# Kernel tuning notes

Hardware: AMD Instinct MI355X
Metric: run time of the kernel (lower is better)

The kernel has to match this reference:

```python
import jax, jax.numpy as jnp
import numpy as np

N_NODES = 100000
N_EDGES = 100000
D = 256
N_SIDE = 2  # rel_list = [side_a, side_b, rel_c, rel_d]
N_REL = 2


def setup_inputs() -> dict:
    key = jax.random.key(0)
    ks = jax.random.split(key, 7)
    h = jax.random.normal(ks[0], (N_NODES, D), dtype=jnp.float32)
    src_idx = jax.random.randint(ks[1], (N_SIDE + N_REL, N_EDGES), 0, N_NODES)
    dst_idx = jax.random.randint(ks[2], (N_SIDE + N_REL, N_EDGES), 0, N_NODES)
    # shared bilinear matrix R (nn.Linear(D, D, bias=False): y = x @ R_W.T)
    R_W = jax.random.normal(ks[3], (D, D), dtype=jnp.float32) * (1.0 / np.sqrt(D))
    # per-'side*' diagonal parameters (xavier over [D,1] then squeeze)
    d_side = jax.random.normal(ks[4], (N_SIDE, D), dtype=jnp.float32)
    # per-regular-relation Linear weights (with bias)
    W_rel = jax.random.normal(ks[5], (N_REL, D, D), dtype=jnp.float32) * (1.0 / np.sqrt(D))
    b_rel = jax.random.normal(ks[6], (N_REL, D), dtype=jnp.float32) * 0.01
    return {"h": h, "src_idx": src_idx, "dst_idx": dst_idx,
            "R_W": R_W, "d_side": d_side, "W_rel": W_rel, "b_rel": b_rel}


def reference(h, src_idx, dst_idx, R_W, d_side, W_rel, b_rel):
    # --- 'side*' edge types: score = (((h_u * d) @ R_W.T) * d) . h_v ---
    hu_s = h[src_idx[:N_SIDE]]            # [S, E, D] gather
    hv_s = h[dst_idx[:N_SIDE]]            # [S, E, D]
    lft = hu_s * d_side[:, None, :]       # [S, E, D]
    lft = jnp.einsum('sed,fd->sef', lft, R_W)  # Linear, no bias
    lft = lft * d_side[:, None, :]
    score_side = jnp.einsum('sed,sed->se', lft, hv_s)  # [S, E]

    # --- regular edge types: score = (h_u @ W.T + b) . h_v ---
    hu_r = h[src_idx[N_SIDE:]]            # [R, E, D]
    hv_r = h[dst_idx[N_SIDE:]]            # [R, E, D]
    lft_r = jnp.einsum('red,rfd->ref', hu_r, W_rel) + b_rel[:, None, :]
    score_rel = jnp.einsum('red,red->re', lft_r, hv_r)  # [R, E]

    return jnp.concatenate([score_side, score_rel], axis=0)  # [S+R, E]
```

## Files before the change

### kernel.cpp

```cpp
#include <hip/hip_runtime.h>
#include <stdint.h>

#define NNODES 100000
#define NEDGES 100000
#define DIM    256
#define NCH    4
#define ET     64
#define NT     1563
#define NBX    64
#define RSF    264
#define CONVB  2048

typedef _Float16 f16x8 __attribute__((ext_vector_type(8)));
typedef _Float16 f16x4 __attribute__((ext_vector_type(4)));
typedef float f32x4  __attribute__((ext_vector_type(4)));

__global__ void prep_fused(const float* __restrict__ RW,
                           const float* __restrict__ dside,
                           const float* __restrict__ Wrel,
                           const float* __restrict__ h,
                           _Float16* __restrict__ Bh, _Float16* __restrict__ Bl,
                           _Float16* __restrict__ H16) {
    if (blockIdx.x < 128) {
        int t = blockIdx.x * blockDim.x + threadIdx.x;
        int lane = t & 63;
        int ft   = (t >> 6) & 15;
        int kc   = (t >> 10) & 7;
        int c    = t >> 13;
        int quad = lane >> 4, col = lane & 15;
        int f     = ft * 16 + col;
        int kbase = kc * 32 + quad * 8;

        f16x8 vh, vl;
#pragma unroll
        for (int j = 0; j < 8; ++j) {
            int k = kbase + j;
            float val;
            if (c < 2) {
                val = dside[c * DIM + f] * RW[f * DIM + k] * dside[c * DIM + k];
            } else {
                val = Wrel[(size_t)(c - 2) * DIM * DIM + f * DIM + k];
            }
            _Float16 hi = (_Float16)val;
            vh[j] = hi;
            vl[j] = (_Float16)(val - (float)hi);
        }
        ((f16x8*)Bh)[t] = vh;
        ((f16x8*)Bl)[t] = vl;
    } else {
        const int total4 = NNODES * DIM / 4;
        const int stride = CONVB * 256;
        int i = (blockIdx.x - 128) * 256 + (int)threadIdx.x;
        const f32x4* s4 = (const f32x4*)h;
        f16x4* d4 = (f16x4*)H16;
        for (; i + stride < total4; i += 2 * stride) {
            f32x4 a = s4[i];
            f32x4 b = s4[i + stride];
            f16x4 oa, ob;
#pragma unroll
            for (int j = 0; j < 4; ++j) { oa[j] = (_Float16)a[j]; ob[j] = (_Float16)b[j]; }
            d4[i] = oa; d4[i + stride] = ob;
        }
        if (i < total4) {
            f32x4 a = s4[i];
            f16x4 o;
#pragma unroll
            for (int j = 0; j < 4; ++j) o[j] = (_Float16)a[j];
            d4[i] = o;
        }
    }
}

__device__ __forceinline__ float dpp_reduce16(float s) {
    union { float f; int i; } u, v;
    u.f = s; v.i = __builtin_amdgcn_update_dpp(0, u.i, 0xB1,  0xF, 0xF, true); s += v.f;
    u.f = s; v.i = __builtin_amdgcn_update_dpp(0, u.i, 0x4E,  0xF, 0xF, true); s += v.f;
    u.f = s; v.i = __builtin_amdgcn_update_dpp(0, u.i, 0x141, 0xF, 0xF, true); s += v.f;
    u.f = s; v.i = __builtin_amdgcn_update_dpp(0, u.i, 0x140, 0xF, 0xF, true); s += v.f;
    return s;
}

__global__ __launch_bounds__(512, 1)
void edge_kernel(const _Float16* __restrict__ H16,
                 const int* __restrict__ src_idx,
                 const int* __restrict__ dst_idx,
                 const float* __restrict__ brel,
                 const _Float16* __restrict__ Bh_sw,
                 const _Float16* __restrict__ Bl_sw,
                 float* __restrict__ out) {
    const int c    = blockIdx.y;
    const int tid  = threadIdx.x;
    const int w    = tid >> 6;
    const int lane = tid & 63;
    const int quad = lane >> 4, col = lane & 15;

    __shared__ __align__(16) _Float16 s_a[ET * RSF];
    __shared__ __align__(16) _Float16 s_v[ET * RSF];
    __shared__ float red[8][ET];

    f16x8 Bh_r[8][2], Bl_r[8][2];
    {
        const f16x8* bh = (const f16x8*)Bh_sw;
        const f16x8* bl = (const f16x8*)Bl_sw;
#pragma unroll
        for (int kc = 0; kc < 8; ++kc)
#pragma unroll
            for (int ftl = 0; ftl < 2; ++ftl) {
                int o = ((c * 8 + kc) * 16 + (w * 2 + ftl)) * 64 + lane;
                Bh_r[kc][ftl] = bh[o];
                Bl_r[kc][ftl] = bl[o];
            }
    }
#pragma unroll
    for (int kc = 0; kc < 8; ++kc)
#pragma unroll
        for (int ftl = 0; ftl < 2; ++ftl)
            asm volatile("" : "+v"(Bh_r[kc][ftl]), "+v"(Bl_r[kc][ftl]));

    float bias[2];
#pragma unroll
    for (int ftl = 0; ftl < 2; ++ftl) {
        int f = (w * 2 + ftl) * 16 + col;
        bias[ftl] = (c >= 2) ? brel[(size_t)(c - 2) * DIM + f] : 0.f;
    }

    const int  j8   = lane & 7;
    const bool isV  = (lane & 8) != 0;
    const int* ibase = (isV ? dst_idx : src_idx) + (size_t)c * NEDGES;

    auto loadpack = [&](int t) -> int {
        int e = t * ET + w * 8 + j8;
        if (e >= NEDGES) e = NEDGES - 1;
        return ibase[e];
    };

    const int t0 = blockIdx.x;
    f16x4 pA[8], pV[8];
    {
        int ip = loadpack(t0);
#pragma unroll
        for (int i = 0; i < 8; ++i) {
            int ia = __shfl(ip, i, 64);
            int iv = __shfl(ip, 8 + i, 64);
            pA[i] = *(const f16x4*)(H16 + (size_t)ia * DIM + lane * 4);
            pV[i] = *(const f16x4*)(H16 + (size_t)iv * DIM + lane * 4);
        }
    }
    int ipk0 = 0, ipk1 = 0;
    if (t0 + NBX < NT) ipk1 = loadpack(t0 + NBX);

    auto body = [&](int t, int& ipkUse, int& ipkLoad) {
#pragma unroll
        for (int i = 0; i < 8; ++i) {
            int lr = w * 8 + i;
            *(f16x4*)&s_a[lr * RSF + lane * 4] = pA[i];
            *(f16x4*)&s_v[lr * RSF + lane * 4] = pV[i];
        }
        __syncthreads();

        if (t + 2 * NBX < NT) ipkLoad = loadpack(t + 2 * NBX);
        if (t + NBX < NT) {
#pragma unroll
            for (int i = 0; i < 8; ++i) {
                int ia = __shfl(ipkUse, i, 64);
                int iv = __shfl(ipkUse, 8 + i, 64);
                pA[i] = *(const f16x4*)(H16 + (size_t)ia * DIM + lane * 4);
                pV[i] = *(const f16x4*)(H16 + (size_t)iv * DIM + lane * 4);
            }
        }

        f32x4 acc[4][2];
#pragma unroll
        for (int mt = 0; mt < 4; ++mt)
#pragma unroll
            for (int ftl = 0; ftl < 2; ++ftl) acc[mt][ftl] = (f32x4){0.f, 0.f, 0.f, 0.f};

#pragma unroll
        for (int kc = 0; kc < 8; ++kc) {
            f16x8 A[4];
#pragma unroll
            for (int mt = 0; mt < 4; ++mt)
                A[mt] = *(const f16x8*)&s_a[(mt * 16 + col) * RSF + kc * 32 + quad * 8];
#pragma unroll
            for (int ftl = 0; ftl < 2; ++ftl) {
#pragma unroll
                for (int mt = 0; mt < 4; ++mt)
                    acc[mt][ftl] = __builtin_amdgcn_mfma_f32_16x16x32_f16(A[mt], Bh_r[kc][ftl], acc[mt][ftl], 0, 0, 0);
#pragma unroll
                for (int mt = 0; mt < 4; ++mt)
                    acc[mt][ftl] = __builtin_amdgcn_mfma_f32_16x16x32_f16(A[mt], Bl_r[kc][ftl], acc[mt][ftl], 0, 0, 0);
            }
        }

        float psum[4][4];
#pragma unroll
        for (int mt = 0; mt < 4; ++mt) {
#pragma unroll
            for (int r = 0; r < 4; ++r) {
                int el = mt * 16 + quad * 4 + r;
                float s = 0.f;
#pragma unroll
                for (int ftl = 0; ftl < 2; ++ftl) {
                    int f = (w * 2 + ftl) * 16 + col;
                    float v = (float)s_v[el * RSF + f];
                    s += (acc[mt][ftl][r] + bias[ftl]) * v;
                }
                psum[mt][r] = dpp_reduce16(s);
            }
        }
        if (col == 0) {
#pragma unroll
            for (int mt = 0; mt < 4; ++mt)
#pragma unroll
                for (int r = 0; r < 4; ++r)
                    red[w][mt * 16 + quad * 4 + r] = psum[mt][r];
        }
        __syncthreads();

        if (tid < ET) {
            int e = t * ET + tid;
            if (e < NEDGES) {
                float s = 0.f;
#pragma unroll
                for (int i = 0; i < 8; ++i) s += red[i][tid];
                out[(size_t)c * NEDGES + e] = s;
            }
        }
    };

    int t = t0;
    while (true) {
        body(t, ipk1, ipk0);
        t += NBX; if (t >= NT) break;
        body(t, ipk0, ipk1);
        t += NBX; if (t >= NT) break;
    }
}

extern "C" void kernel_launch(void* const* d_in, const int* in_sizes, int n_in,
                              void* d_out, int out_size, void* d_ws, size_t ws_size,
                              hipStream_t stream) {
    const float* hmat  = (const float*)d_in[0];
    const int*   src   = (const int*)d_in[1];
    const int*   dst   = (const int*)d_in[2];
    const float* RW    = (const float*)d_in[3];
    const float* dside = (const float*)d_in[4];
    const float* Wrel  = (const float*)d_in[5];
    const float* brel  = (const float*)d_in[6];
    float* out = (float*)d_out;

    const size_t nB = (size_t)NCH * DIM * DIM;
    _Float16* Bh  = (_Float16*)d_ws;
    _Float16* Bl  = Bh + nB;
    _Float16* H16 = Bl + nB;

    prep_fused<<<dim3(128 + CONVB), dim3(256), 0, stream>>>(
        RW, dside, Wrel, hmat, Bh, Bl, H16);

    dim3 grid(NBX, NCH);
    edge_kernel<<<grid, dim3(512), 0, stream>>>(H16, src, dst, brel, Bh, Bl, out);
}
```

Baseline: 277.7 us.

## Double-buffer edge tiles and replace block reduction with atomic accumulation

The edge kernel now alternates between two LDS tile buffers, which drops one of the two block-wide barriers per iteration. The cross-wave reduction through shared memory is replaced by per-wave float atomicAdd into the output, which the prep kernel now zeroes first. Index broadcasts use readlane instead of shfl. The tradeoff is more global atomic traffic, a nondeterministic summation order, and twice the LDS footprint.

```diff
diff --git a/kernel.cpp b/kernel.cpp
--- a/kernel.cpp
+++ b/kernel.cpp
@@ -10,6 +10,7 @@
 #define NBX    64
 #define RSF    264
 #define CONVB  2048
+#define ZEROB  391
 
 typedef _Float16 f16x8 __attribute__((ext_vector_type(8)));
 typedef _Float16 f16x4 __attribute__((ext_vector_type(4)));
@@ -20,7 +21,8 @@
                            const float* __restrict__ Wrel,
                            const float* __restrict__ h,
                            _Float16* __restrict__ Bh, _Float16* __restrict__ Bl,
-                           _Float16* __restrict__ H16) {
+                           _Float16* __restrict__ H16,
+                           float* __restrict__ out) {
     if (blockIdx.x < 128) {
         int t = blockIdx.x * blockDim.x + threadIdx.x;
         int lane = t & 63;
@@ -47,10 +49,14 @@
         }
         ((f16x8*)Bh)[t] = vh;
         ((f16x8*)Bl)[t] = vl;
+    } else if (blockIdx.x < 128 + ZEROB) {
+        int i4 = (blockIdx.x - 128) * 256 + (int)threadIdx.x;
+        if (i4 < NCH * NEDGES / 4)
+            ((f32x4*)out)[i4] = (f32x4){0.f, 0.f, 0.f, 0.f};
     } else {
         const int total4 = NNODES * DIM / 4;
         const int stride = CONVB * 256;
-        int i = (blockIdx.x - 128) * 256 + (int)threadIdx.x;
+        int i = (blockIdx.x - 128 - ZEROB) * 256 + (int)threadIdx.x;
         const f32x4* s4 = (const f32x4*)h;
         f16x4* d4 = (f16x4*)H16;
         for (; i + stride < total4; i += 2 * stride) {
@@ -94,9 +100,10 @@
     const int lane = tid & 63;
     const int quad = lane >> 4, col = lane & 15;
 
-    __shared__ __align__(16) _Float16 s_a[ET * RSF];
-    __shared__ __align__(16) _Float16 s_v[ET * RSF];
-    __shared__ float red[8][ET];
+    __shared__ __align__(16) _Float16 s_a0[ET * RSF];
+    __shared__ __align__(16) _Float16 s_v0[ET * RSF];
+    __shared__ __align__(16) _Float16 s_a1[ET * RSF];
+    __shared__ __align__(16) _Float16 s_v1[ET * RSF];
 
     f16x8 Bh_r[8][2], Bl_r[8][2];
     {
@@ -140,8 +147,8 @@
         int ip = loadpack(t0);
 #pragma unroll
         for (int i = 0; i < 8; ++i) {
-            int ia = __shfl(ip, i, 64);
-            int iv = __shfl(ip, 8 + i, 64);
+            int ia = __builtin_amdgcn_readlane(ip, i);
+            int iv = __builtin_amdgcn_readlane(ip, 8 + i);
             pA[i] = *(const f16x4*)(H16 + (size_t)ia * DIM + lane * 4);
             pV[i] = *(const f16x4*)(H16 + (size_t)iv * DIM + lane * 4);
         }
@@ -149,26 +156,27 @@
     int ipk0 = 0, ipk1 = 0;
     if (t0 + NBX < NT) ipk1 = loadpack(t0 + NBX);
 
-    auto body = [&](int t, int& ipkUse, int& ipkLoad) {
+    auto body = [&](int t, _Float16* sa, _Float16* sv, int& ipkUse, int& ipkLoad) {
 #pragma unroll
         for (int i = 0; i < 8; ++i) {
             int lr = w * 8 + i;
-            *(f16x4*)&s_a[lr * RSF + lane * 4] = pA[i];
-            *(f16x4*)&s_v[lr * RSF + lane * 4] = pV[i];
-        }
-        __syncthreads();
+            *(f16x4*)&sa[lr * RSF + lane * 4] = pA[i];
+            *(f16x4*)&sv[lr * RSF + lane * 4] = pV[i];
+        }
 
         if (t + 2 * NBX < NT) ipkLoad = loadpack(t + 2 * NBX);
         if (t + NBX < NT) {
 #pragma unroll
             for (int i = 0; i < 8; ++i) {
-                int ia = __shfl(ipkUse, i, 64);
-                int iv = __shfl(ipkUse, 8 + i, 64);
+                int ia = __builtin_amdgcn_readlane(ipkUse, i);
+                int iv = __builtin_amdgcn_readlane(ipkUse, 8 + i);
                 pA[i] = *(const f16x4*)(H16 + (size_t)ia * DIM + lane * 4);
                 pV[i] = *(const f16x4*)(H16 + (size_t)iv * DIM + lane * 4);
             }
         }
 
+        __syncthreads();
+
         f32x4 acc[4][2];
 #pragma unroll
         for (int mt = 0; mt < 4; ++mt)
@@ -180,7 +188,7 @@
             f16x8 A[4];
 #pragma unroll
             for (int mt = 0; mt < 4; ++mt)
-                A[mt] = *(const f16x8*)&s_a[(mt * 16 + col) * RSF + kc * 32 + quad * 8];
+                A[mt] = *(const f16x8*)&sa[(mt * 16 + col) * RSF + kc * 32 + quad * 8];
 #pragma unroll
             for (int ftl = 0; ftl < 2; ++ftl) {
 #pragma unroll
@@ -192,9 +200,9 @@
             }
         }
 
-        float psum[4][4];
 #pragma unroll
         for (int mt = 0; mt < 4; ++mt) {
+            float ps[4];
 #pragma unroll
             for (int r = 0; r < 4; ++r) {
                 int el = mt * 16 + quad * 4 + r;
@@ -202,37 +210,27 @@
 #pragma unroll
                 for (int ftl = 0; ftl < 2; ++ftl) {
                     int f = (w * 2 + ftl) * 16 + col;
-                    float v = (float)s_v[el * RSF + f];
+                    float v = (float)sv[el * RSF + f];
                     s += (acc[mt][ftl][r] + bias[ftl]) * v;
                 }
-                psum[mt][r] = dpp_reduce16(s);
-            }
-        }
-        if (col == 0) {
-#pragma unroll
-            for (int mt = 0; mt < 4; ++mt)
-#pragma unroll
-                for (int r = 0; r < 4; ++r)
-                    red[w][mt * 16 + quad * 4 + r] = psum[mt][r];
-        }
-        __syncthreads();
-
-        if (tid < ET) {
-            int e = t * ET + tid;
-            if (e < NEDGES) {
-                float s = 0.f;
-#pragma unroll
-                for (int i = 0; i < 8; ++i) s += red[i][tid];
-                out[(size_t)c * NEDGES + e] = s;
+                ps[r] = dpp_reduce16(s);
+            }
+            if (col == 0) {
+#pragma unroll
+                for (int r = 0; r < 4; ++r) {
+                    int e = t * ET + mt * 16 + quad * 4 + r;
+                    if (e < NEDGES)
+                        atomicAdd(&out[(size_t)c * NEDGES + e], ps[r]);
+                }
             }
         }
     };
 
     int t = t0;
     while (true) {
-        body(t, ipk1, ipk0);
+        body(t, s_a0, s_v0, ipk1, ipk0);
         t += NBX; if (t >= NT) break;
-        body(t, ipk0, ipk1);
+        body(t, s_a1, s_v1, ipk0, ipk1);
         t += NBX; if (t >= NT) break;
     }
 }
@@ -254,8 +252,8 @@
     _Float16* Bl  = Bh + nB;
     _Float16* H16 = Bl + nB;
 
-    prep_fused<<<dim3(128 + CONVB), dim3(256), 0, stream>>>(
-        RW, dside, Wrel, hmat, Bh, Bl, H16);
+    prep_fused<<<dim3(128 + ZEROB + CONVB), dim3(256), 0, stream>>>(
+        RW, dside, Wrel, hmat, Bh, Bl, H16, out);
 
     dim3 grid(NBX, NCH);
     edge_kernel<<<grid, dim3(512), 0, stream>>>(H16, src, dst, brel, Bh, Bl, out);
```

New measurement: 290.3 us. 4.6% more time.

## Double-buffer LDS tiles with XOR swizzle and 16-byte gathers

Applied to the files above, without the earlier changes.

Replaces the padded single LDS buffer with two unpadded buffers that use an XOR swizzle, so the next tile is written into the alternate buffer after the MFMA loop. Row gathers become 16-byte loads (two rows per wave per step) addressed with readlane instead of 8-byte loads through shuffles. The MFMA section is wrapped in s_setprio. The aim is to overlap global gathers with compute, widen loads and avoid LDS bank conflicts. The cost is twice the LDS footprint and added swizzle index arithmetic.

```diff
diff --git a/kernel.cpp b/kernel.cpp
--- a/kernel.cpp
+++ b/kernel.cpp
@@ -8,7 +8,6 @@
 #define ET     64
 #define NT     1563
 #define NBX    64
-#define RSF    264
 #define CONVB  2048
 
 typedef _Float16 f16x8 __attribute__((ext_vector_type(8)));
@@ -93,9 +92,10 @@
     const int w    = tid >> 6;
     const int lane = tid & 63;
     const int quad = lane >> 4, col = lane & 15;
-
-    __shared__ __align__(16) _Float16 s_a[ET * RSF];
-    __shared__ __align__(16) _Float16 s_v[ET * RSF];
+    const int c7   = col & 7;
+
+    __shared__ __align__(16) _Float16 s_a[2][ET * DIM];
+    __shared__ __align__(16) _Float16 s_v[2][ET * DIM];
     __shared__ float red[8][ET];
 
     f16x8 Bh_r[8][2], Bl_r[8][2];
@@ -134,40 +134,49 @@
         return ibase[e];
     };
 
+    const int halfsel = lane >> 5;
+    const int p31     = lane & 31;
+
+    f16x8 rA[4], rV[4];
+    auto loadTileRegs = [&](int ip) {
+#pragma unroll
+        for (int i = 0; i < 4; ++i) {
+            int a0 = __builtin_amdgcn_readlane(ip, 2 * i);
+            int a1 = __builtin_amdgcn_readlane(ip, 2 * i + 1);
+            int v0 = __builtin_amdgcn_readlane(ip, 8 + 2 * i);
+            int v1 = __builtin_amdgcn_readlane(ip, 8 + 2 * i + 1);
+            int idxA = halfsel ? a1 : a0;
+            int idxV = halfsel ? v1 : v0;
+            int r7  = (2 * i + halfsel) & 7;
+            int lsl = (p31 ^ r7) << 3;
+            rA[i] = *(const f16x8*)(H16 + (size_t)idxA * DIM + lsl);
+            rV[i] = *(const f16x8*)(H16 + (size_t)idxV * DIM + lsl);
+        }
+    };
+    auto writeTileRegs = [&](_Float16* sa, _Float16* sv) {
+#pragma unroll
+        for (int i = 0; i < 4; ++i) {
+            int dst = (w * 8 + 2 * i + halfsel) * DIM + p31 * 8;
+            *(f16x8*)&sa[dst] = rA[i];
+            *(f16x8*)&sv[dst] = rV[i];
+        }
+    };
+
     const int t0 = blockIdx.x;
-    f16x4 pA[8], pV[8];
-    {
-        int ip = loadpack(t0);
-#pragma unroll
-        for (int i = 0; i < 8; ++i) {
-            int ia = __shfl(ip, i, 64);
-            int iv = __shfl(ip, 8 + i, 64);
-            pA[i] = *(const f16x4*)(H16 + (size_t)ia * DIM + lane * 4);
-            pV[i] = *(const f16x4*)(H16 + (size_t)iv * DIM + lane * 4);
-        }
-    }
+    loadTileRegs(loadpack(t0));
+    writeTileRegs(s_a[0], s_v[0]);
     int ipk0 = 0, ipk1 = 0;
     if (t0 + NBX < NT) ipk1 = loadpack(t0 + NBX);
 
-    auto body = [&](int t, int& ipkUse, int& ipkLoad) {
-#pragma unroll
-        for (int i = 0; i < 8; ++i) {
-            int lr = w * 8 + i;
-            *(f16x4*)&s_a[lr * RSF + lane * 4] = pA[i];
-            *(f16x4*)&s_v[lr * RSF + lane * 4] = pV[i];
-        }
+    auto body = [&](int t, int par, int& ipkUse, int& ipkLoad) {
+        _Float16* sa = s_a[par];
+        _Float16* sv = s_v[par];
+
         __syncthreads();
 
         if (t + 2 * NBX < NT) ipkLoad = loadpack(t + 2 * NBX);
-        if (t + NBX < NT) {
-#pragma unroll
-            for (int i = 0; i < 8; ++i) {
-                int ia = __shfl(ipkUse, i, 64);
-                int iv = __shfl(ipkUse, 8 + i, 64);
-                pA[i] = *(const f16x4*)(H16 + (size_t)ia * DIM + lane * 4);
-                pV[i] = *(const f16x4*)(H16 + (size_t)iv * DIM + lane * 4);
-            }
-        }
+        const bool havenext = (t + NBX < NT);
+        if (havenext) loadTileRegs(ipkUse);
 
         f32x4 acc[4][2];
 #pragma unroll
@@ -175,12 +184,13 @@
 #pragma unroll
             for (int ftl = 0; ftl < 2; ++ftl) acc[mt][ftl] = (f32x4){0.f, 0.f, 0.f, 0.f};
 
+        __builtin_amdgcn_s_setprio(1);
 #pragma unroll
         for (int kc = 0; kc < 8; ++kc) {
             f16x8 A[4];
 #pragma unroll
             for (int mt = 0; mt < 4; ++mt)
-                A[mt] = *(const f16x8*)&s_a[(mt * 16 + col) * RSF + kc * 32 + quad * 8];
+                A[mt] = *(const f16x8*)&sa[(mt * 16 + col) * DIM + (((kc * 4 + quad) ^ c7) << 3)];
 #pragma unroll
             for (int ftl = 0; ftl < 2; ++ftl) {
 #pragma unroll
@@ -191,6 +201,9 @@
                     acc[mt][ftl] = __builtin_amdgcn_mfma_f32_16x16x32_f16(A[mt], Bl_r[kc][ftl], acc[mt][ftl], 0, 0, 0);
             }
         }
+        __builtin_amdgcn_s_setprio(0);
+
+        if (havenext) writeTileRegs(s_a[par ^ 1], s_v[par ^ 1]);
 
         float psum[4][4];
 #pragma unroll
@@ -202,7 +215,8 @@
 #pragma unroll
                 for (int ftl = 0; ftl < 2; ++ftl) {
                     int f = (w * 2 + ftl) * 16 + col;
-                    float v = (float)s_v[el * RSF + f];
+                    int phys = (f >> 3) ^ (el & 7);
+                    float v = (float)sv[el * DIM + phys * 8 + (f & 7)];
                     s += (acc[mt][ftl][r] + bias[ftl]) * v;
                 }
                 psum[mt][r] = dpp_reduce16(s);
@@ -230,9 +244,9 @@
 
     int t = t0;
     while (true) {
-        body(t, ipk1, ipk0);
+        body(t, 0, ipk1, ipk0);
         t += NBX; if (t >= NT) break;
-        body(t, ipk0, ipk1);
+        body(t, 1, ipk0, ipk1);
         t += NBX; if (t >= NT) break;
     }
 }
```

New measurement: 326.8 us. 1.18x slower.
